# Kernel optimization log

Measured on AMD Instinct MI355X. Metric: run time of the kernel, lower is better.

## Reference

```python
import jax, jax.numpy as jnp
import numpy as np

DIM = 3072
HEADS = 24
HEAD_DIM = 128
SEQ = 4096
BATCH = 1
EPS = 1e-6


def setup_inputs() -> dict:
    key = jax.random.key(0)
    ks = jax.random.split(key, 12)
    s = 1.0 / np.sqrt(DIM)
    return {
        "hidden_states": jax.random.normal(ks[0], (BATCH, SEQ, DIM), dtype=jnp.float32),
        "cos": jax.random.uniform(ks[1], (SEQ, HEAD_DIM), dtype=jnp.float32, minval=-1.0, maxval=1.0),
        "sin": jax.random.uniform(ks[2], (SEQ, HEAD_DIM), dtype=jnp.float32, minval=-1.0, maxval=1.0),
        "Wq": jax.random.normal(ks[3], (DIM, HEADS * HEAD_DIM), dtype=jnp.float32) * s,
        "bq": jax.random.normal(ks[4], (HEADS * HEAD_DIM,), dtype=jnp.float32) * 0.02,
        "Wk": jax.random.normal(ks[5], (DIM, HEADS * HEAD_DIM), dtype=jnp.float32) * s,
        "bk": jax.random.normal(ks[6], (HEADS * HEAD_DIM,), dtype=jnp.float32) * 0.02,
        "Wv": jax.random.normal(ks[7], (DIM, HEADS * HEAD_DIM), dtype=jnp.float32) * s,
        "bv": jax.random.normal(ks[8], (HEADS * HEAD_DIM,), dtype=jnp.float32) * 0.02,
        "gq": jnp.ones((HEAD_DIM,), dtype=jnp.float32),
        "gk": jnp.ones((HEAD_DIM,), dtype=jnp.float32),
    }


def _rms_norm(x, g):
    # RMSNorm over last dim (head_dim), learnable scale g
    var = jnp.mean(jnp.square(x), axis=-1, keepdims=True)
    return x * jax.lax.rsqrt(var + EPS) * g


def _apply_rope(x, cos, sin):
    # x: [B, S, H, D]; cos/sin: [S, D]. Interleaved-pair rotation (Flux style).
    xr = x.reshape(*x.shape[:-1], HEAD_DIM // 2, 2)
    x_rot = jnp.stack((-xr[..., 1], xr[..., 0]), axis=-1).reshape(x.shape)
    c = cos[None, :, None, :]
    s = sin[None, :, None, :]
    return x * c + x_rot * s


def reference(hidden_states, cos, sin, Wq, bq, Wk, bk, Wv, bv, gq, gk):
    B, S, _ = hidden_states.shape
    q = (hidden_states @ Wq + bq).reshape(B, S, HEADS, HEAD_DIM)
    k = (hidden_states @ Wk + bk).reshape(B, S, HEADS, HEAD_DIM)
    v = (hidden_states @ Wv + bv).reshape(B, S, HEADS, HEAD_DIM)
    q = _apply_rope(_rms_norm(q, gq), cos, sin)
    k = _apply_rope(_rms_norm(k, gk), cos, sin)
    scale = 1.0 / jnp.sqrt(jnp.asarray(HEAD_DIM, dtype=q.dtype))
    scores = jnp.einsum("bqhd,bkhd->bhqk", q, k) * scale  # [B, H, S, S]
    probs = jax.nn.softmax(scores, axis=-1)
    out = jnp.einsum("bhqk,bkhd->bqhd", probs, v)  # [B, S, H, D]
    return out.reshape(B, S, HEADS * HEAD_DIM)
```

## Files before the change

kernel.cpp:

```cpp
#include <hip/hip_runtime.h>
#include <hip/hip_bf16.h>
#include <stdint.h>

#define DIM 3072
#define SEQ 4096
#define NH 24
#define HD 128

typedef __hip_bfloat16 bf16;
typedef __bf16 bfv8 __attribute__((ext_vector_type(8)));
typedef float f32x4 __attribute__((ext_vector_type(4)));
typedef float f32x16 __attribute__((ext_vector_type(16)));
typedef unsigned short us4 __attribute__((ext_vector_type(4)));
typedef unsigned short us8 __attribute__((ext_vector_type(8)));

template <int N> struct ic { static constexpr int value = N; };

__device__ __forceinline__ void async16(void* lds, const void* g) {
  __builtin_amdgcn_global_load_lds((const __attribute__((address_space(1))) void*)g,
                                   (__attribute__((address_space(3))) void*)lds, 16, 0, 0);
}

__device__ __forceinline__ unsigned short f2bf(float f) {
  unsigned int u = __builtin_bit_cast(unsigned int, f);
  u += 0x7fffu + ((u >> 16) & 1u);
  return (unsigned short)(u >> 16);
}
__device__ __forceinline__ float bf2f(unsigned short b) {
  return __builtin_bit_cast(float, (unsigned int)b << 16);
}
__device__ __forceinline__ unsigned int cvtpk(float lo, float hi) {
  unsigned int r;
  asm("v_cvt_pk_bf16_f32 %0, %1, %2" : "=v"(r) : "v"(lo), "v"(hi));
  return r;
}
__device__ __forceinline__ void pl32swap(unsigned int& a, unsigned int& b) {
  asm volatile("v_permlane32_swap_b32 %0, %1" : "+v"(a), "+v"(b));
}
#if __has_builtin(__builtin_amdgcn_exp2f)
__device__ __forceinline__ float fexp2(float x) { return __builtin_amdgcn_exp2f(x); }
#else
__device__ __forceinline__ float fexp2(float x) { return exp2f(x); }
#endif

#define MFMA16(a, b, c) __builtin_amdgcn_mfma_f32_16x16x32_bf16((a), (b), (c), 0, 0, 0)
#define MFMA32(a, b, c) __builtin_amdgcn_mfma_f32_32x32x16_bf16((a), (b), (c), 0, 0, 0)

__global__ __launch_bounds__(256) void k_cast(const float4* __restrict__ in,
                                              us4* __restrict__ o, int n4) {
  int i = blockIdx.x * 256 + threadIdx.x;
  if (i >= n4) return;
  float4 v = in[i];
  us4 r;
  r.x = f2bf(v.x); r.y = f2bf(v.y); r.z = f2bf(v.z); r.w = f2bf(v.w);
  o[i] = r;
}

__global__ __launch_bounds__(256) void k_transW(const float* __restrict__ W0,
    const float* __restrict__ W1, const float* __restrict__ W2,
    unsigned short* __restrict__ T0, unsigned short* __restrict__ T1,
    unsigned short* __restrict__ T2) {
  int z = blockIdx.z;
  const float* W = (z == 0) ? W0 : (z == 1) ? W1 : W2;
  unsigned short* T = (z == 0) ? T0 : (z == 1) ? T1 : T2;
  int kb = blockIdx.y * 64;
  int nb = blockIdx.x * 64;
  __shared__ float tile[64 * 64];
  int t = threadIdx.x;
#pragma unroll
  for (int p = 0; p < 4; ++p) {
    int cid = p * 256 + t;
    int row = cid >> 4, c4 = cid & 15;
    int slot = (c4 + (row >> 3)) & 15;
    float4 v = *(const float4*)&W[(size_t)(kb + row) * DIM + nb + c4 * 4];
    *(float4*)&tile[row * 64 + slot * 4] = v;
  }
  __syncthreads();
#pragma unroll
  for (int p = 0; p < 2; ++p) {
    int cid = p * 256 + t;
    int nl = cid >> 3, c8 = cid & 7;
    us8 o;
#pragma unroll
    for (int j = 0; j < 8; ++j) {
      int k = c8 * 8 + j;
      int slot = ((nl >> 2) + (k >> 3)) & 15;
      o[j] = f2bf(tile[k * 64 + slot * 4 + (nl & 3)]);
    }
    *(us8*)&T[(size_t)(nb + nl) * DIM + kb + c8 * 8] = o;
  }
}

__global__ __launch_bounds__(256, 3) void k_gemm(const unsigned short* __restrict__ A,
    const unsigned short* __restrict__ B0, const unsigned short* __restrict__ B1,
    const unsigned short* __restrict__ B2, const float* __restrict__ c0,
    const float* __restrict__ c1, const float* __restrict__ c2,
    unsigned short* __restrict__ o0, unsigned short* __restrict__ o1,
    unsigned short* __restrict__ o2) {
  const int b = blockIdx.x;
  const int yb = b % 32;
  const int r2b = b / 32;
  const int xb = r2b % 24;
  const int z = r2b / 24;
  const unsigned short* Bt = (z == 0) ? B0 : (z == 1) ? B1 : B2;
  const float* bias = (z == 0) ? c0 : (z == 1) ? c1 : c2;
  unsigned short* outp = (z == 0) ? o0 : (z == 1) ? o1 : o2;
  const int nb = xb * 128;
  const int mb = yb * 128;
  const int t = threadIdx.x;
  const int w = t >> 6, l = t & 63;
  const int wr = w >> 1, wc = w & 1;
  const int lq = l & 15, lg = l >> 4;
  __shared__ unsigned short lA[128 * 64];
  __shared__ unsigned short lB[128 * 64];
  f32x4 acc[4][4];
#pragma unroll
  for (int i = 0; i < 4; ++i)
#pragma unroll
    for (int j = 0; j < 4; ++j) acc[i][j] = (f32x4){0.f, 0.f, 0.f, 0.f};

  for (int kb = 0; kb < DIM; kb += 64) {
    __syncthreads();
#pragma unroll
    for (int r = 0; r < 4; ++r) {
      int row = (w * 4 + r) * 8 + (l >> 3);
      int sl = (l & 7) ^ (row & 7);
      async16(&lA[(w * 4 + r) * 512], A + (size_t)(mb + row) * DIM + kb + sl * 8);
      async16(&lB[(w * 4 + r) * 512], Bt + (size_t)(nb + row) * DIM + kb + sl * 8);
    }
    __syncthreads();
#pragma unroll
    for (int kc = 0; kc < 2; ++kc) {
      bfv8 af[4], bfv[4];
#pragma unroll
      for (int mf = 0; mf < 4; ++mf) {
        int row = wr * 64 + mf * 16 + lq;
        af[mf] = *(const bfv8*)&lA[row * 64 + (((kc * 4 + lg) ^ (row & 7)) * 8)];
      }
#pragma unroll
      for (int nf = 0; nf < 4; ++nf) {
        int row = wc * 64 + nf * 16 + lq;
        bfv[nf] = *(const bfv8*)&lB[row * 64 + (((kc * 4 + lg) ^ (row & 7)) * 8)];
      }
#pragma unroll
      for (int mf = 0; mf < 4; ++mf)
#pragma unroll
        for (int nf = 0; nf < 4; ++nf)
          acc[mf][nf] = MFMA16(af[mf], bfv[nf], acc[mf][nf]);
    }
  }
#pragma unroll
  for (int nf = 0; nf < 4; ++nf) {
    int n = nb + wc * 64 + nf * 16 + lq;
    float bv_ = bias[n];
    int hh = n >> 7, dd = n & 127;
    unsigned short* obase = outp + (size_t)hh * SEQ * HD + dd;
#pragma unroll
    for (int mf = 0; mf < 4; ++mf) {
      int srow = mb + wr * 64 + mf * 16 + lg * 4;
#pragma unroll
      for (int r = 0; r < 4; ++r)
        obase[(size_t)(srow + r) * HD] = f2bf(acc[mf][nf][r] + bv_);
    }
  }
}

__global__ __launch_bounds__(256) void k_rmsrope(unsigned short* __restrict__ qb,
    unsigned short* __restrict__ kbuf, const float* __restrict__ cosT,
    const float* __restrict__ sinT, const float* __restrict__ gq,
    const float* __restrict__ gk) {
  int rowid = blockIdx.x * 4 + (threadIdx.x >> 6);
  int l = threadIdx.x & 63;
  int which = (rowid >= NH * SEQ) ? 1 : 0;
  int r2 = which ? rowid - NH * SEQ : rowid;
  int hh = r2 >> 12;
  int s = r2 & 4095;
  unsigned short* base = (which ? kbuf : qb) + ((size_t)hh * SEQ + s) * HD + 2 * l;
  const float* g = which ? gk : gq;
  unsigned int u = *(const unsigned int*)base;
  float x0 = bf2f((unsigned short)(u & 0xffffu));
  float x1 = bf2f((unsigned short)(u >> 16));
  float ss = x0 * x0 + x1 * x1;
#pragma unroll
  for (int o = 1; o < 64; o <<= 1) ss += __shfl_xor(ss, o);
  float rr = rsqrtf(ss * (1.0f / 128.0f) + 1e-6f);
  int d0 = 2 * l;
  float c0v = cosT[s * HD + d0], c1v = cosT[s * HD + d0 + 1];
  float s0v = sinT[s * HD + d0], s1v = sinT[s * HD + d0 + 1];
  float y0 = x0 * rr * g[d0];
  float y1 = x1 * rr * g[d0 + 1];
  float o0 = y0 * c0v - y1 * s0v;
  float o1 = y1 * c1v + y0 * s1v;
  if (!which) { o0 *= 0.1275174373f; o1 *= 0.1275174373f; }
  *(unsigned int*)base = (unsigned int)f2bf(o0) | ((unsigned int)f2bf(o1) << 16);
}

__global__ __launch_bounds__(256) void k_transV(const unsigned short* __restrict__ vb,
                                                unsigned short* __restrict__ vt) {
  int hh = blockIdx.y;
  int sb = blockIdx.x * 64;
  __shared__ unsigned short tile[64 * 128];
  int t = threadIdx.x;
#pragma unroll
  for (int p = 0; p < 4; ++p) {
    int cid = p * 256 + t;
    int row = cid >> 4, c = cid & 15;
    int slot = (c + (row >> 3)) & 15;
    us8 v = *(const us8*)&vb[((size_t)hh * SEQ + sb + row) * HD + c * 8];
    *(us8*)&tile[row * 128 + slot * 8] = v;
  }
  __syncthreads();
#pragma unroll
  for (int p = 0; p < 4; ++p) {
    int cid = p * 256 + t;
    int d = cid >> 3, c8 = cid & 7;
    us8 o;
#pragma unroll
    for (int j = 0; j < 8; ++j) {
      int s = c8 * 8 + j;
      int slot = ((d >> 3) + (s >> 3)) & 15;
      o[j] = tile[s * 128 + slot * 8 + (d & 7)];
    }
    *(us8*)&vt[((size_t)hh * HD + d) * SEQ + sb + c8 * 8] = o;
  }
}

__global__ __launch_bounds__(256, 2) void k_attn(const unsigned short* __restrict__ qg,
    const unsigned short* __restrict__ kg, const unsigned short* __restrict__ vtg,
    float* __restrict__ outp) {
  const int bflat = blockIdx.x;
  const int h = bflat % 24;
  const int qb0 = (bflat / 24) * 128;
  const int t = threadIdx.x;
  const int w = t >> 6, l = t & 63;
  const int l31 = l & 31, hi = l >> 5;

  __shared__ unsigned short lKf[2 * 8192];
  __shared__ unsigned short lVf[2 * 8192];

  bfv8 qf[8];
  {
    const unsigned short* qrow = qg + ((size_t)h * SEQ + qb0 + w * 32 + l31) * HD + hi * 8;
#pragma unroll
    for (int ks = 0; ks < 8; ++ks) qf[ks] = *(const bfv8*)(qrow + ks * 16);
  }

  int kidx[8], vidx[4][2];
#pragma unroll
  for (int ks = 0; ks < 8; ++ks)
    kidx[ks] = l31 * 128 + (((ks * 2 + hi) ^ (l31 & 7) ^ ((l31 >> 3) & 1)) * 8);
#pragma unroll
  for (int dt = 0; dt < 4; ++dt)
#pragma unroll
    for (int ksub = 0; ksub < 2; ++ksub)
      vidx[dt][ksub] =
          (dt * 32 + l31) * 32 + (((ksub * 2 + hi) ^ (l31 & 3) ^ ((l31 >> 2) & 3)) * 8);

  const unsigned short *kp0, *kp1, *vp0, *vp1;
  {
    int kr0 = w * 4 + (l >> 4), kr1 = 16 + kr0;
    kp0 = kg + ((size_t)h * SEQ + kr0) * HD + (((l & 15) ^ (kr0 & 7) ^ ((kr0 >> 3) & 1)) * 8);
    kp1 = kg + ((size_t)h * SEQ + kr1) * HD + (((l & 15) ^ (kr1 & 7) ^ ((kr1 >> 3) & 1)) * 8);
    int vr0 = w * 16 + (l >> 2), vr1 = 64 + vr0;
    vp0 = vtg + ((size_t)h * HD + vr0) * SEQ + (((l & 3) ^ (vr0 & 3) ^ ((vr0 >> 2) & 3)) * 8);
    vp1 = vtg + ((size_t)h * HD + vr1) * SEQ + (((l & 3) ^ (vr1 & 3) ^ ((vr1 >> 2) & 3)) * 8);
  }

#define STAGE(B)                                                              \
  do {                                                                        \
    async16(&lKf[(B) * 8192 + w * 512], kp0);                                 \
    async16(&lKf[(B) * 8192 + 2048 + w * 512], kp1);                          \
    async16(&lKf[(B) * 8192 + 4096 + w * 512], kp0 + 32 * HD);                \
    async16(&lKf[(B) * 8192 + 6144 + w * 512], kp1 + 32 * HD);                \
    async16(&lVf[(B) * 8192 + w * 512], vp0);                                 \
    async16(&lVf[(B) * 8192 + 2048 + w * 512], vp1);                          \
    async16(&lVf[(B) * 8192 + 4096 + w * 512], vp0 + 32);                     \
    async16(&lVf[(B) * 8192 + 6144 + w * 512], vp1 + 32);                     \
    kp0 += 64 * HD; kp1 += 64 * HD; vp0 += 64; vp1 += 64;                     \
  } while (0)

  f32x16 oacc[4];
#pragma unroll
  for (int dt = 0; dt < 4; ++dt)
#pragma unroll
    for (int r = 0; r < 16; ++r) oacc[dt][r] = 0.f;
  float l_run = 0.f;

  STAGE(0);

  auto phase = [&](auto bufc, auto stagec) {
    constexpr int CUR = decltype(bufc)::value;
    constexpr int DOSTAGE = decltype(stagec)::value;
    asm volatile("s_waitcnt vmcnt(0)" ::: "memory");
    __builtin_amdgcn_s_barrier();
    __builtin_amdgcn_sched_barrier(0);
    if constexpr (DOSTAGE) STAGE(CUR ^ 1);
    __builtin_amdgcn_sched_barrier(0);

    f32x16 sa, sb;
#pragma unroll
    for (int r = 0; r < 16; ++r) { sa[r] = 0.f; sb[r] = 0.f; }
    __builtin_amdgcn_s_setprio(1);
#pragma unroll
    for (int ks = 0; ks < 8; ++ks) {
      bfv8 kfa = *(const bfv8*)&lKf[CUR * 8192 + kidx[ks]];
      bfv8 kfb = *(const bfv8*)&lKf[CUR * 8192 + 4096 + kidx[ks]];
      sa = MFMA32(kfa, qf[ks], sa);
      sb = MFMA32(kfb, qf[ks], sb);
    }
    __builtin_amdgcn_s_setprio(0);

#pragma unroll
    for (int r = 0; r < 16; ++r) { sa[r] = fexp2(sa[r]); sb[r] = fexp2(sb[r]); }
    {
      float a0 = (sa[0] + sa[1]) + (sa[2] + sa[3]);
      float a1 = (sa[4] + sa[5]) + (sa[6] + sa[7]);
      float a2 = (sa[8] + sa[9]) + (sa[10] + sa[11]);
      float a3 = (sa[12] + sa[13]) + (sa[14] + sa[15]);
      float b0 = (sb[0] + sb[1]) + (sb[2] + sb[3]);
      float b1 = (sb[4] + sb[5]) + (sb[6] + sb[7]);
      float b2 = (sb[8] + sb[9]) + (sb[10] + sb[11]);
      float b3 = (sb[12] + sb[13]) + (sb[14] + sb[15]);
      l_run += ((a0 + a1) + (a2 + a3)) + ((b0 + b1) + (b2 + b3));
    }

    bfv8 paA[2], paB[2];
    {
      unsigned int a0 = cvtpk(sa[0], sa[1]), a1 = cvtpk(sa[2], sa[3]);
      unsigned int b0 = cvtpk(sa[4], sa[5]), b1 = cvtpk(sa[6], sa[7]);
      unsigned int c0 = cvtpk(sa[8], sa[9]), c1 = cvtpk(sa[10], sa[11]);
      unsigned int d0 = cvtpk(sa[12], sa[13]), d1 = cvtpk(sa[14], sa[15]);
      pl32swap(a0, b0); pl32swap(a1, b1); pl32swap(c0, d0); pl32swap(c1, d1);
      paA[0] = __builtin_bit_cast(bfv8, make_uint4(a0, a1, b0, b1));
      paA[1] = __builtin_bit_cast(bfv8, make_uint4(c0, c1, d0, d1));
      a0 = cvtpk(sb[0], sb[1]); a1 = cvtpk(sb[2], sb[3]);
      b0 = cvtpk(sb[4], sb[5]); b1 = cvtpk(sb[6], sb[7]);
      c0 = cvtpk(sb[8], sb[9]); c1 = cvtpk(sb[10], sb[11]);
      d0 = cvtpk(sb[12], sb[13]); d1 = cvtpk(sb[14], sb[15]);
      pl32swap(a0, b0); pl32swap(a1, b1); pl32swap(c0, d0); pl32swap(c1, d1);
      paB[0] = __builtin_bit_cast(bfv8, make_uint4(a0, a1, b0, b1));
      paB[1] = __builtin_bit_cast(bfv8, make_uint4(c0, c1, d0, d1));
    }

    __builtin_amdgcn_s_setprio(1);
#pragma unroll
    for (int dt = 0; dt < 4; ++dt) {
#pragma unroll
      for (int ksub = 0; ksub < 2; ++ksub) {
        bfv8 vfa = *(const bfv8*)&lVf[CUR * 8192 + vidx[dt][ksub]];
        oacc[dt] = MFMA32(paA[ksub], vfa, oacc[dt]);
      }
#pragma unroll
      for (int ksub = 0; ksub < 2; ++ksub) {
        bfv8 vfb = *(const bfv8*)&lVf[CUR * 8192 + 4096 + vidx[dt][ksub]];
        oacc[dt] = MFMA32(paB[ksub], vfb, oacc[dt]);
      }
    }
    __builtin_amdgcn_s_setprio(0);
  };

  for (int it = 0; it < 31; ++it) {
    phase(ic<0>{}, ic<1>{});
    phase(ic<1>{}, ic<1>{});
  }
  phase(ic<0>{}, ic<1>{});
  phase(ic<1>{}, ic<0>{});

  l_run += __shfl_xor(l_run, 32);
  float linv = 1.0f / l_run;
#pragma unroll
  for (int r = 0; r < 16; ++r) {
    int qr = (r & 3) + 8 * (r >> 2) + 4 * hi;
    float lr = __shfl(linv, qr);
    float* orow = outp + (size_t)(qb0 + w * 32 + qr) * DIM + h * HD;
#pragma unroll
    for (int dt = 0; dt < 4; ++dt) orow[dt * 32 + l31] = oacc[dt][r] * lr;
  }
#undef STAGE
}

extern "C" void kernel_launch(void* const* d_in, const int* in_sizes, int n_in,
                              void* d_out, int out_size, void* d_ws, size_t ws_size,
                              hipStream_t stream) {
  const float* hs = (const float*)d_in[0];
  const float* cosT = (const float*)d_in[1];
  const float* sinT = (const float*)d_in[2];
  const float* Wq = (const float*)d_in[3];
  const float* bq = (const float*)d_in[4];
  const float* Wk = (const float*)d_in[5];
  const float* bk = (const float*)d_in[6];
  const float* Wv = (const float*)d_in[7];
  const float* bv = (const float*)d_in[8];
  const float* gq = (const float*)d_in[9];
  const float* gk = (const float*)d_in[10];
  float* out = (float*)d_out;

  char* ws = (char*)d_ws;
  const size_t SZ_HS = (size_t)SEQ * DIM * 2;
  const size_t SZ_W = (size_t)DIM * DIM * 2;
  const size_t SZ_HEAD = (size_t)NH * SEQ * HD * 2;
  unsigned short* hsb = (unsigned short*)ws;               ws += SZ_HS;
  unsigned short* WqT = (unsigned short*)ws;               ws += SZ_W;
  unsigned short* WkT = (unsigned short*)ws;               ws += SZ_W;
  unsigned short* WvT = (unsigned short*)ws;               ws += SZ_W;
  unsigned short* q_b = (unsigned short*)ws;               ws += SZ_HEAD;
  unsigned short* k_b = (unsigned short*)ws;               ws += SZ_HEAD;
  unsigned short* v_b = (unsigned short*)ws;               ws += SZ_HEAD;
  unsigned short* vtr = (unsigned short*)ws;               ws += SZ_HEAD;

  int n4 = SEQ * DIM / 4;
  k_cast<<<dim3(n4 / 256), dim3(256), 0, stream>>>((const float4*)hs, (us4*)hsb, n4);
  k_transW<<<dim3(48, 48, 3), dim3(256), 0, stream>>>(Wq, Wk, Wv, WqT, WkT, WvT);
  k_gemm<<<dim3(2304), dim3(256), 0, stream>>>(hsb, WqT, WkT, WvT, bq, bk, bv,
                                               q_b, k_b, v_b);
  k_rmsrope<<<dim3(2 * NH * SEQ / 4), dim3(256), 0, stream>>>(q_b, k_b, cosT, sinT, gq, gk);
  k_transV<<<dim3(64, 24), dim3(256), 0, stream>>>(v_b, vtr);
  k_attn<<<dim3(768), dim3(256), 0, stream>>>(q_b, k_b, vtr, out);
}
```

Before: 542.2 us.

## Rewrite QKV GEMM with 256x256 tiles and double-buffered async LDS pipeline

Replaces the 128x128 single-buffered QKV projection GEMM with a 256x256 tile per 512-thread block. The new kernel uses double-buffered LDS split into k-halves and issues async global-to-LDS loads interleaved with MFMA phases, using explicit barriers, vmcnt waits and setprio. The aim is to hide global load latency behind compute and raise arithmetic intensity per LDS byte. The cost is more LDS and registers per block, and only 576 blocks, which may leave the last wave unevenly spread across CUs.

```diff
diff --git a/kernel.cpp b/kernel.cpp
--- a/kernel.cpp
+++ b/kernel.cpp
@@ -91,78 +91,176 @@
   }
 }
 
-__global__ __launch_bounds__(256, 3) void k_gemm(const unsigned short* __restrict__ A,
+__global__ __launch_bounds__(512, 2) void k_gemm(const unsigned short* __restrict__ A,
     const unsigned short* __restrict__ B0, const unsigned short* __restrict__ B1,
     const unsigned short* __restrict__ B2, const float* __restrict__ c0,
     const float* __restrict__ c1, const float* __restrict__ c2,
     unsigned short* __restrict__ o0, unsigned short* __restrict__ o1,
     unsigned short* __restrict__ o2) {
-  const int b = blockIdx.x;
-  const int yb = b % 32;
-  const int r2b = b / 32;
-  const int xb = r2b % 24;
-  const int z = r2b / 24;
+  const int z = blockIdx.z;
   const unsigned short* Bt = (z == 0) ? B0 : (z == 1) ? B1 : B2;
   const float* bias = (z == 0) ? c0 : (z == 1) ? c1 : c2;
   unsigned short* outp = (z == 0) ? o0 : (z == 1) ? o1 : o2;
-  const int nb = xb * 128;
-  const int mb = yb * 128;
-  const int t = threadIdx.x;
-  const int w = t >> 6, l = t & 63;
-  const int wr = w >> 1, wc = w & 1;
+  const int nb = blockIdx.x * 256;
+  const int mb = blockIdx.y * 256;
+  const int tid = threadIdx.x;
+  const int w = tid >> 6, l = tid & 63;
+  const int wm = w >> 2, wn = w & 3;
   const int lq = l & 15, lg = l >> 4;
-  __shared__ unsigned short lA[128 * 64];
-  __shared__ unsigned short lB[128 * 64];
-  f32x4 acc[4][4];
-#pragma unroll
-  for (int i = 0; i < 4; ++i)
+
+  __shared__ unsigned short lA[2 * 2 * 8192];
+  __shared__ unsigned short lB[2 * 2 * 8192];
+
+  const int rowAb = wm * 128 + lq;
+  const int aswz = (rowAb >> 1) & 3;
+  const int aoff0 = rowAb * 32 + ((lg ^ aswz) * 8);
+  const int rowBb = wn * 64 + lq;
+  const int bswz = (rowBb >> 1) & 3;
+  const int boff0 = rowBb * 32 + ((lg ^ bswz) * 8);
+
+  const int r0 = tid >> 2, c40 = tid & 3;
+  const int r1 = (512 + tid) >> 2, c41 = tid & 3;
+  const int sw0 = (r0 >> 1) & 3, sw1 = (r1 >> 1) & 3;
+  const unsigned short* aK0i0 = A + (size_t)(mb + r0) * DIM + ((c40 ^ sw0) * 8);
+  const unsigned short* aK0i1 = A + (size_t)(mb + r1) * DIM + ((c41 ^ sw1) * 8);
+  const unsigned short* aK1i0 = A + (size_t)(mb + r0) * DIM + 32 + ((c40 ^ sw0) * 8);
+  const unsigned short* aK1i1 = A + (size_t)(mb + r1) * DIM + 32 + ((c41 ^ sw1) * 8);
+  const unsigned short* bK0i0 = Bt + (size_t)(nb + r0) * DIM + ((c40 ^ sw0) * 8);
+  const unsigned short* bK0i1 = Bt + (size_t)(nb + r1) * DIM + ((c41 ^ sw1) * 8);
+  const unsigned short* bK1i0 = Bt + (size_t)(nb + r0) * DIM + 32 + ((c40 ^ sw0) * 8);
+  const unsigned short* bK1i1 = Bt + (size_t)(nb + r1) * DIM + 32 + ((c41 ^ sw1) * 8);
+  const int dst0 = w * 512, dst1 = 4096 + w * 512;
+
+#define SA0(B)                                                           \
+  do {                                                                   \
+    async16(&lA[(B) * 16384 + dst0], aK0i0); aK0i0 += 64;                \
+    async16(&lA[(B) * 16384 + dst1], aK0i1); aK0i1 += 64;                \
+  } while (0)
+#define SB0(B)                                                           \
+  do {                                                                   \
+    async16(&lB[(B) * 16384 + dst0], bK0i0); bK0i0 += 64;                \
+    async16(&lB[(B) * 16384 + dst1], bK0i1); bK0i1 += 64;                \
+  } while (0)
+#define SA1(B)                                                           \
+  do {                                                                   \
+    async16(&lA[(B) * 16384 + 8192 + dst0], aK1i0); aK1i0 += 64;         \
+    async16(&lA[(B) * 16384 + 8192 + dst1], aK1i1); aK1i1 += 64;         \
+  } while (0)
+#define SB1(B)                                                           \
+  do {                                                                   \
+    async16(&lB[(B) * 16384 + 8192 + dst0], bK1i0); bK1i0 += 64;         \
+    async16(&lB[(B) * 16384 + 8192 + dst1], bK1i1); bK1i1 += 64;         \
+  } while (0)
+
+  f32x4 acc[8][4];
+#pragma unroll
+  for (int i = 0; i < 8; ++i)
 #pragma unroll
     for (int j = 0; j < 4; ++j) acc[i][j] = (f32x4){0.f, 0.f, 0.f, 0.f};
 
-  for (int kb = 0; kb < DIM; kb += 64) {
-    __syncthreads();
-#pragma unroll
-    for (int r = 0; r < 4; ++r) {
-      int row = (w * 4 + r) * 8 + (l >> 3);
-      int sl = (l & 7) ^ (row & 7);
-      async16(&lA[(w * 4 + r) * 512], A + (size_t)(mb + row) * DIM + kb + sl * 8);
-      async16(&lB[(w * 4 + r) * 512], Bt + (size_t)(nb + row) * DIM + kb + sl * 8);
-    }
-    __syncthreads();
-#pragma unroll
-    for (int kc = 0; kc < 2; ++kc) {
-      bfv8 af[4], bfv[4];
-#pragma unroll
-      for (int mf = 0; mf < 4; ++mf) {
-        int row = wr * 64 + mf * 16 + lq;
-        af[mf] = *(const bfv8*)&lA[row * 64 + (((kc * 4 + lg) ^ (row & 7)) * 8)];
-      }
-#pragma unroll
-      for (int nf = 0; nf < 4; ++nf) {
-        int row = wc * 64 + nf * 16 + lq;
-        bfv[nf] = *(const bfv8*)&lB[row * 64 + (((kc * 4 + lg) ^ (row & 7)) * 8)];
-      }
-#pragma unroll
-      for (int mf = 0; mf < 4; ++mf)
-#pragma unroll
-        for (int nf = 0; nf < 4; ++nf)
-          acc[mf][nf] = MFMA16(af[mf], bfv[nf], acc[mf][nf]);
-    }
-  }
+  SA0(0); SB0(0); SA1(0); SB1(0); SA0(1); SB0(1);
+  asm volatile("s_waitcnt vmcnt(4)" ::: "memory");
+  __builtin_amdgcn_s_barrier();
+  __builtin_amdgcn_sched_barrier(0);
+
+  auto tileG = [&](auto bufc, auto kh1c, auto kh0c, auto waitc) {
+    constexpr int C = decltype(bufc)::value;
+    constexpr int DO1 = decltype(kh1c)::value;
+    constexpr int DO0 = decltype(kh0c)::value;
+    constexpr int WN = decltype(waitc)::value;
+    bfv8 aF[4], bF[4];
+#pragma unroll
+    for (int nf = 0; nf < 4; ++nf)
+      bF[nf] = *(const bfv8*)&lB[C * 16384 + boff0 + nf * 512];
+#pragma unroll
+    for (int mf = 0; mf < 4; ++mf)
+      aF[mf] = *(const bfv8*)&lA[C * 16384 + aoff0 + mf * 512];
+    if constexpr (DO1) SA1(C ^ 1);
+    __builtin_amdgcn_s_barrier();
+    __builtin_amdgcn_sched_barrier(0);
+    __builtin_amdgcn_s_setprio(1);
+#pragma unroll
+    for (int mf = 0; mf < 4; ++mf)
+#pragma unroll
+      for (int nf = 0; nf < 4; ++nf) acc[mf][nf] = MFMA16(aF[mf], bF[nf], acc[mf][nf]);
+    __builtin_amdgcn_s_setprio(0);
+    __builtin_amdgcn_s_barrier();
+#pragma unroll
+    for (int mf = 0; mf < 4; ++mf)
+      aF[mf] = *(const bfv8*)&lA[C * 16384 + aoff0 + (mf + 4) * 512];
+    if constexpr (DO1) SB1(C ^ 1);
+    __builtin_amdgcn_s_barrier();
+    __builtin_amdgcn_sched_barrier(0);
+    __builtin_amdgcn_s_setprio(1);
+#pragma unroll
+    for (int mf = 0; mf < 4; ++mf)
+#pragma unroll
+      for (int nf = 0; nf < 4; ++nf)
+        acc[mf + 4][nf] = MFMA16(aF[mf], bF[nf], acc[mf + 4][nf]);
+    __builtin_amdgcn_s_setprio(0);
+    __builtin_amdgcn_s_barrier();
+#pragma unroll
+    for (int nf = 0; nf < 4; ++nf)
+      bF[nf] = *(const bfv8*)&lB[C * 16384 + 8192 + boff0 + nf * 512];
+#pragma unroll
+    for (int mf = 0; mf < 4; ++mf)
+      aF[mf] = *(const bfv8*)&lA[C * 16384 + 8192 + aoff0 + mf * 512];
+    if constexpr (DO0) SA0(C);
+    __builtin_amdgcn_s_barrier();
+    __builtin_amdgcn_sched_barrier(0);
+    __builtin_amdgcn_s_setprio(1);
+#pragma unroll
+    for (int mf = 0; mf < 4; ++mf)
+#pragma unroll
+      for (int nf = 0; nf < 4; ++nf) acc[mf][nf] = MFMA16(aF[mf], bF[nf], acc[mf][nf]);
+    __builtin_amdgcn_s_setprio(0);
+    __builtin_amdgcn_s_barrier();
+#pragma unroll
+    for (int mf = 0; mf < 4; ++mf)
+      aF[mf] = *(const bfv8*)&lA[C * 16384 + 8192 + aoff0 + (mf + 4) * 512];
+    if constexpr (DO0) SB0(C);
+    __builtin_amdgcn_s_barrier();
+    __builtin_amdgcn_sched_barrier(0);
+    __builtin_amdgcn_s_setprio(1);
+#pragma unroll
+    for (int mf = 0; mf < 4; ++mf)
+#pragma unroll
+      for (int nf = 0; nf < 4; ++nf)
+        acc[mf + 4][nf] = MFMA16(aF[mf], bF[nf], acc[mf + 4][nf]);
+    __builtin_amdgcn_s_setprio(0);
+    if constexpr (WN == 4)
+      asm volatile("s_waitcnt vmcnt(4)" ::: "memory");
+    else if constexpr (WN == 0)
+      asm volatile("s_waitcnt vmcnt(0)" ::: "memory");
+    __builtin_amdgcn_s_barrier();
+    __builtin_amdgcn_sched_barrier(0);
+  };
+
+  for (int it = 0; it < 23; ++it) {
+    tileG(ic<0>{}, ic<1>{}, ic<1>{}, ic<4>{});
+    tileG(ic<1>{}, ic<1>{}, ic<1>{}, ic<4>{});
+  }
+  tileG(ic<0>{}, ic<1>{}, ic<0>{}, ic<0>{});
+  tileG(ic<1>{}, ic<0>{}, ic<0>{}, ic<-1>{});
+
 #pragma unroll
   for (int nf = 0; nf < 4; ++nf) {
-    int n = nb + wc * 64 + nf * 16 + lq;
+    int n = nb + wn * 64 + nf * 16 + lq;
     float bv_ = bias[n];
     int hh = n >> 7, dd = n & 127;
     unsigned short* obase = outp + (size_t)hh * SEQ * HD + dd;
 #pragma unroll
-    for (int mf = 0; mf < 4; ++mf) {
-      int srow = mb + wr * 64 + mf * 16 + lg * 4;
+    for (int mf = 0; mf < 8; ++mf) {
+      int srow = mb + wm * 128 + mf * 16 + lg * 4;
 #pragma unroll
       for (int r = 0; r < 4; ++r)
         obase[(size_t)(srow + r) * HD] = f2bf(acc[mf][nf][r] + bv_);
     }
   }
+#undef SA0
+#undef SB0
+#undef SA1
+#undef SB1
 }
 
 __global__ __launch_bounds__(256) void k_rmsrope(unsigned short* __restrict__ qb,
@@ -411,8 +509,8 @@
   int n4 = SEQ * DIM / 4;
   k_cast<<<dim3(n4 / 256), dim3(256), 0, stream>>>((const float4*)hs, (us4*)hsb, n4);
   k_transW<<<dim3(48, 48, 3), dim3(256), 0, stream>>>(Wq, Wk, Wv, WqT, WkT, WvT);
-  k_gemm<<<dim3(2304), dim3(256), 0, stream>>>(hsb, WqT, WkT, WvT, bq, bk, bv,
-                                               q_b, k_b, v_b);
+  k_gemm<<<dim3(12, 16, 3), dim3(512), 0, stream>>>(hsb, WqT, WkT, WvT, bq, bk, bv,
+                                                    q_b, k_b, v_b);
   k_rmsrope<<<dim3(2 * NH * SEQ / 4), dim3(256), 0, stream>>>(q_b, k_b, cosT, sinT, gq, gk);
   k_transV<<<dim3(64, 24), dim3(256), 0, stream>>>(v_b, vtr);
   k_attn<<<dim3(768), dim3(256), 0, stream>>>(q_b, k_b, vtr, out);
```

New measurement: 568.5 us. 4.9% more time.

## Fuse RMSNorm and RoPE into the QKV projection GEMM epilogue

Applied to the files above, without the earlier changes.

Removes the separate k_rmsrope kernel and applies bias, per-head RMSNorm, RoPE and the query scale in the GEMM epilogue. Each block's 128-column N tile is exactly one head, so row sums of squares are reduced with lane shuffles and combined across the two column-warps through a small LDS buffer. This avoids a full read-modify-write pass over the Q and K buffers plus one launch. In exchange the epilogue does more work, including strided cos/sin loads and a block barrier, and holds extra registers.

```diff
diff --git a/kernel.cpp b/kernel.cpp
--- a/kernel.cpp
+++ b/kernel.cpp
@@ -95,6 +95,8 @@
     const unsigned short* __restrict__ B0, const unsigned short* __restrict__ B1,
     const unsigned short* __restrict__ B2, const float* __restrict__ c0,
     const float* __restrict__ c1, const float* __restrict__ c2,
+    const float* __restrict__ cosT, const float* __restrict__ sinT,
+    const float* __restrict__ gq, const float* __restrict__ gk,
     unsigned short* __restrict__ o0, unsigned short* __restrict__ o1,
     unsigned short* __restrict__ o2) {
   const int b = blockIdx.x;
@@ -113,6 +115,7 @@
   const int lq = l & 15, lg = l >> 4;
   __shared__ unsigned short lA[128 * 64];
   __shared__ unsigned short lB[128 * 64];
+  __shared__ float lds_sq[128 * 2];
   f32x4 acc[4][4];
 #pragma unroll
   for (int i = 0; i < 4; ++i)
@@ -149,50 +152,83 @@
           acc[mf][nf] = MFMA16(af[mf], bfv[nf], acc[mf][nf]);
     }
   }
-#pragma unroll
-  for (int nf = 0; nf < 4; ++nf) {
-    int n = nb + wc * 64 + nf * 16 + lq;
-    float bv_ = bias[n];
-    int hh = n >> 7, dd = n & 127;
-    unsigned short* obase = outp + (size_t)hh * SEQ * HD + dd;
-#pragma unroll
-    for (int mf = 0; mf < 4; ++mf) {
-      int srow = mb + wr * 64 + mf * 16 + lg * 4;
+
+  float bv4[4];
+#pragma unroll
+  for (int nf = 0; nf < 4; ++nf) bv4[nf] = bias[nb + wc * 64 + nf * 16 + lq];
+#pragma unroll
+  for (int mf = 0; mf < 4; ++mf)
+#pragma unroll
+    for (int nf = 0; nf < 4; ++nf)
+#pragma unroll
+      for (int r = 0; r < 4; ++r) acc[mf][nf][r] += bv4[nf];
+
+  const int hh = nb >> 7;
+  unsigned short* obase0 = outp + (size_t)hh * SEQ * HD;
+
+  if (z == 2) {
+#pragma unroll
+    for (int nf = 0; nf < 4; ++nf) {
+      int dd = wc * 64 + nf * 16 + lq;
+#pragma unroll
+      for (int mf = 0; mf < 4; ++mf) {
+        int srow = mb + wr * 64 + mf * 16 + lg * 4;
+#pragma unroll
+        for (int r = 0; r < 4; ++r)
+          obase0[(size_t)(srow + r) * HD + dd] = f2bf(acc[mf][nf][r]);
+      }
+    }
+    return;
+  }
+
+  float psum[4][4];
+#pragma unroll
+  for (int mf = 0; mf < 4; ++mf)
+#pragma unroll
+    for (int r = 0; r < 4; ++r) {
+      float p = acc[mf][0][r] * acc[mf][0][r];
+      p += acc[mf][1][r] * acc[mf][1][r];
+      p += acc[mf][2][r] * acc[mf][2][r];
+      p += acc[mf][3][r] * acc[mf][3][r];
+      p += __shfl_xor(p, 1);
+      p += __shfl_xor(p, 2);
+      p += __shfl_xor(p, 4);
+      p += __shfl_xor(p, 8);
+      psum[mf][r] = p;
+    }
+  if (lq == 0) {
+#pragma unroll
+    for (int mf = 0; mf < 4; ++mf)
 #pragma unroll
       for (int r = 0; r < 4; ++r)
-        obase[(size_t)(srow + r) * HD] = f2bf(acc[mf][nf][r] + bv_);
-    }
-  }
-}
-
-__global__ __launch_bounds__(256) void k_rmsrope(unsigned short* __restrict__ qb,
-    unsigned short* __restrict__ kbuf, const float* __restrict__ cosT,
-    const float* __restrict__ sinT, const float* __restrict__ gq,
-    const float* __restrict__ gk) {
-  int rowid = blockIdx.x * 4 + (threadIdx.x >> 6);
-  int l = threadIdx.x & 63;
-  int which = (rowid >= NH * SEQ) ? 1 : 0;
-  int r2 = which ? rowid - NH * SEQ : rowid;
-  int hh = r2 >> 12;
-  int s = r2 & 4095;
-  unsigned short* base = (which ? kbuf : qb) + ((size_t)hh * SEQ + s) * HD + 2 * l;
-  const float* g = which ? gk : gq;
-  unsigned int u = *(const unsigned int*)base;
-  float x0 = bf2f((unsigned short)(u & 0xffffu));
-  float x1 = bf2f((unsigned short)(u >> 16));
-  float ss = x0 * x0 + x1 * x1;
-#pragma unroll
-  for (int o = 1; o < 64; o <<= 1) ss += __shfl_xor(ss, o);
-  float rr = rsqrtf(ss * (1.0f / 128.0f) + 1e-6f);
-  int d0 = 2 * l;
-  float c0v = cosT[s * HD + d0], c1v = cosT[s * HD + d0 + 1];
-  float s0v = sinT[s * HD + d0], s1v = sinT[s * HD + d0 + 1];
-  float y0 = x0 * rr * g[d0];
-  float y1 = x1 * rr * g[d0 + 1];
-  float o0 = y0 * c0v - y1 * s0v;
-  float o1 = y1 * c1v + y0 * s1v;
-  if (!which) { o0 *= 0.1275174373f; o1 *= 0.1275174373f; }
-  *(unsigned int*)base = (unsigned int)f2bf(o0) | ((unsigned int)f2bf(o1) << 16);
+        lds_sq[(wr * 64 + mf * 16 + lg * 4 + r) * 2 + wc] = psum[mf][r];
+  }
+  __syncthreads();
+
+  const float* g = (z == 0) ? gq : gk;
+  float gvec[4];
+#pragma unroll
+  for (int nf = 0; nf < 4; ++nf) gvec[nf] = g[wc * 64 + nf * 16 + lq];
+  const float qs = (z == 0) ? 0.1275174373f : 1.0f;
+
+#pragma unroll
+  for (int mf = 0; mf < 4; ++mf)
+#pragma unroll
+    for (int r = 0; r < 4; ++r) {
+      int row = wr * 64 + mf * 16 + lg * 4 + r;
+      float tot = lds_sq[row * 2] + lds_sq[row * 2 + 1];
+      float rrv = rsqrtf(tot * (1.0f / 128.0f) + 1e-6f);
+      int s = mb + row;
+#pragma unroll
+      for (int nf = 0; nf < 4; ++nf) {
+        int dd = wc * 64 + nf * 16 + lq;
+        float y = acc[mf][nf][r] * rrv * gvec[nf];
+        float yp = __shfl_xor(y, 1);
+        float cc = cosT[s * HD + dd], sn = sinT[s * HD + dd];
+        float o = (lq & 1) ? fmaf(yp, sn, y * cc) : fmaf(-yp, sn, y * cc);
+        obase0[(size_t)s * HD + dd] = f2bf(o * qs);
+      }
+    }
 }
 
 __global__ __launch_bounds__(256) void k_transV(const unsigned short* __restrict__ vb,
@@ -412,8 +448,7 @@
   k_cast<<<dim3(n4 / 256), dim3(256), 0, stream>>>((const float4*)hs, (us4*)hsb, n4);
   k_transW<<<dim3(48, 48, 3), dim3(256), 0, stream>>>(Wq, Wk, Wv, WqT, WkT, WvT);
   k_gemm<<<dim3(2304), dim3(256), 0, stream>>>(hsb, WqT, WkT, WvT, bq, bk, bv,
-                                               q_b, k_b, v_b);
-  k_rmsrope<<<dim3(2 * NH * SEQ / 4), dim3(256), 0, stream>>>(q_b, k_b, cosT, sinT, gq, gk);
+                                               cosT, sinT, gq, gk, q_b, k_b, v_b);
   k_transV<<<dim3(64, 24), dim3(256), 0, stream>>>(v_b, vtr);
   k_attn<<<dim3(768), dim3(256), 0, stream>>>(q_b, k_b, vtr, out);
 }
```

Measured after the change: 517.2 us. 1.05x faster.
